# Kernel tuning notes

Measured on AMD Instinct MI355X. Metric: run time of the kernel, lower is better.

Reference implementation:

```python
import jax, jax.numpy as jnp
import numpy as np

B, T, DIM = 4, 2048, 64
NUM_CODES = 512

def setup_inputs() -> dict:
    key = jax.random.key(0)
    k1, k2 = jax.random.split(key)
    inputs = jax.random.normal(k1, (B, T, DIM), dtype=jnp.float32)
    # original init: truncated_normal(mean=0.5, stddev=0) -> constant 0.5; use
    # a real random codebook so argmin is non-degenerate, matching trained state
    lookup_table = jax.random.normal(k2, (NUM_CODES, DIM), dtype=jnp.float32)
    return {"inputs": inputs, "lookup_table": lookup_table}

def reference(inputs, lookup_table):
    # z: [B, T, 1, dim]; table: [1, 1, K, dim] -> diff [B, T, K, dim]
    diff = inputs[..., None, :] - lookup_table[None, None, :, :]
    dist = jnp.linalg.norm(diff, axis=-1)          # [B, T, K]
    k = jnp.argmin(dist, axis=-1)                  # [B, T] int
    z_q = jnp.take(lookup_table, k, axis=0)        # [B, T, dim]
    return (k, z_q)
```

## Files before the change

### kernel.cpp

```cpp
#include <hip/hip_runtime.h>
#include <math.h>


#define NQ      8192
#define VDIM    64
#define NCODES  512
#define QB      32
#define CB      32
#define NCHUNK  (NCODES / CB)

__global__ __launch_bounds__(64, 2) void vq_dist_kernel(
    const float* __restrict__ inp,
    const float* __restrict__ table,
    float* __restrict__ wnorm,
    int* __restrict__ widx)
{
    __shared__ float4 qt[QB * 16];
    __shared__ float4 ct[CB * 16];

    const int l  = threadIdx.x;
    const int bc = blockIdx.x & (NCHUNK - 1);
    const int bq = blockIdx.x >> 4;

    {
        const float4* gq = reinterpret_cast<const float4*>(inp   + (size_t)bq * QB * VDIM);
        const float4* gc = reinterpret_cast<const float4*>(table + (size_t)bc * CB * VDIM);
#pragma unroll
        for (int it = 0; it < 8; ++it) {
            int f  = l + it * 64;
            int r  = f >> 4;
            int kc = f & 15;
            int d  = r * 16 + (kc ^ ((r >> 2) & 7));
            qt[d] = gq[f];
            ct[d] = gc[f];
        }
    }
    __syncthreads();

    const int xq = l & 7;
    const int xc = l >> 3;
    const float4* qb = qt + xq * 4 * 16;
    const float4* cb = ct + xc * 4 * 16;

    float acc[4][4][8];
#pragma unroll
    for (int i = 0; i < 4; ++i)
#pragma unroll
        for (int j = 0; j < 4; ++j)
#pragma unroll
            for (int m = 0; m < 8; ++m) acc[i][j][m] = 0.0f;

#pragma clang loop unroll(disable)
    for (int k = 0; k < 8; ++k) {
        {
            const int kc = 2 * k;
            float4 qv[4], cv[4];
#pragma unroll
            for (int i = 0; i < 4; ++i) qv[i] = qb[i * 16 + (kc ^ xq)];
#pragma unroll
            for (int j = 0; j < 4; ++j) cv[j] = cb[j * 16 + (kc ^ xc)];
#pragma unroll
            for (int i = 0; i < 4; ++i)
#pragma unroll
                for (int j = 0; j < 4; ++j) {
                    float d0 = qv[i].x - cv[j].x;
                    float d1 = qv[i].y - cv[j].y;
                    float d2 = qv[i].z - cv[j].z;
                    float d3 = qv[i].w - cv[j].w;
                    acc[i][j][0] = __builtin_fmaf(d0, d0, acc[i][j][0]);
                    acc[i][j][1] = __builtin_fmaf(d1, d1, acc[i][j][1]);
                    acc[i][j][2] = __builtin_fmaf(d2, d2, acc[i][j][2]);
                    acc[i][j][3] = __builtin_fmaf(d3, d3, acc[i][j][3]);
                }
        }
        {
            const int kc = 2 * k + 1;
            float4 qv[4], cv[4];
#pragma unroll
            for (int i = 0; i < 4; ++i) qv[i] = qb[i * 16 + (kc ^ xq)];
#pragma unroll
            for (int j = 0; j < 4; ++j) cv[j] = cb[j * 16 + (kc ^ xc)];
#pragma unroll
            for (int i = 0; i < 4; ++i)
#pragma unroll
                for (int j = 0; j < 4; ++j) {
                    float d0 = qv[i].x - cv[j].x;
                    float d1 = qv[i].y - cv[j].y;
                    float d2 = qv[i].z - cv[j].z;
                    float d3 = qv[i].w - cv[j].w;
                    acc[i][j][4] = __builtin_fmaf(d0, d0, acc[i][j][4]);
                    acc[i][j][5] = __builtin_fmaf(d1, d1, acc[i][j][5]);
                    acc[i][j][6] = __builtin_fmaf(d2, d2, acc[i][j][6]);
                    acc[i][j][7] = __builtin_fmaf(d3, d3, acc[i][j][7]);
                }
        }
    }

    float bd[4];
    int   bi[4];
#pragma unroll
    for (int i = 0; i < 4; ++i) { bd[i] = INFINITY; bi[i] = 0; }
#pragma unroll
    for (int j = 0; j < 4; ++j) {
#pragma unroll
        for (int i = 0; i < 4; ++i) {
            float s = ((acc[i][j][0] + acc[i][j][1]) + (acc[i][j][2] + acc[i][j][3]))
                    + ((acc[i][j][4] + acc[i][j][5]) + (acc[i][j][6] + acc[i][j][7]));
            float n = sqrtf(s);
            if (n < bd[i]) { bd[i] = n; bi[i] = bc * CB + xc * 4 + j; }
        }
    }

#pragma unroll
    for (int off = 8; off < 64; off <<= 1) {
#pragma unroll
        for (int i = 0; i < 4; ++i) {
            float nd = __shfl_xor(bd[i], off, 64);
            int   ni = __shfl_xor(bi[i], off, 64);
            if (nd < bd[i] || (nd == bd[i] && ni < bi[i])) { bd[i] = nd; bi[i] = ni; }
        }
    }

    if (xc == 0) {
#pragma unroll
        for (int i = 0; i < 4; ++i) {
            wnorm[(size_t)bc * NQ + bq * QB + 4 * l + i] = bd[i];
            widx [(size_t)bc * NQ + bq * QB + 4 * l + i] = bi[i];
        }
    }
}

__global__ __launch_bounds__(256) void vq_finalize_kernel(
    const float* __restrict__ table,
    const float* __restrict__ wnorm,
    const int* __restrict__ widx,
    float* __restrict__ out)
{
    const int gid = blockIdx.x * 256 + threadIdx.x;
    const int q = gid >> 6;
    const int d = gid & 63;

    float best = INFINITY;
    int   bidx = 0;
#pragma unroll
    for (int p = 0; p < NCHUNK; ++p) {
        float n = wnorm[(size_t)p * NQ + q];
        int   i = widx [(size_t)p * NQ + q];
        if (n < best || (n == best && i < bidx)) { best = n; bidx = i; }
    }

    out[NQ + (size_t)q * VDIM + d] = table[(size_t)bidx * VDIM + d];
    if (d == 0) out[q] = (float)bidx;
}

extern "C" void kernel_launch(void* const* d_in, const int* in_sizes, int n_in,
                              void* d_out, int out_size, void* d_ws, size_t ws_size,
                              hipStream_t stream) {
    const float* inp   = (const float*)d_in[0];
    const float* table = (const float*)d_in[1];
    float* out = (float*)d_out;

    float* wnorm = (float*)d_ws;
    int*   widx  = (int*)(wnorm + (size_t)NCHUNK * NQ);

    vq_dist_kernel<<<dim3((NQ / QB) * NCHUNK), dim3(64), 0, stream>>>(inp, table, wnorm, widx);
    vq_finalize_kernel<<<dim3((NQ * VDIM) / 256), dim3(256), 0, stream>>>(table, wnorm, widx, out);
}
```

Baseline: 36.83 us.

## Fuse distance, argmin and gather into one kernel with in-block reduction

Replaces the two-kernel scheme (partial argmin per code chunk written to workspace, then a finalize kernel) with one kernel. Each block handles 16 queries across all 512 codes, split over 4 waves, and reduces the argmin through shuffles and shared memory before gathering codebook rows. This drops the workspace round trip and the second launch. In exchange, the LDS staging is gone and operands are read straight from global memory through cache. The grid also shrinks to 512 blocks, which lowers parallelism.

```diff
diff --git a/kernel.cpp b/kernel.cpp
--- a/kernel.cpp
+++ b/kernel.cpp
@@ -5,114 +5,107 @@
 #define NQ      8192
 #define VDIM    64
 #define NCODES  512
-#define QB      32
-#define CB      32
-#define NCHUNK  (NCODES / CB)
 
-__global__ __launch_bounds__(64, 2) void vq_dist_kernel(
+__global__ __launch_bounds__(256, 2) void vq_fused_kernel(
     const float* __restrict__ inp,
     const float* __restrict__ table,
-    float* __restrict__ wnorm,
-    int* __restrict__ widx)
+    float* __restrict__ out)
 {
-    __shared__ float4 qt[QB * 16];
-    __shared__ float4 ct[CB * 16];
+    __shared__ float red_n[4][16];
+    __shared__ int   red_i[4][16];
+    __shared__ int   kidx[16];
 
-    const int l  = threadIdx.x;
-    const int bc = blockIdx.x & (NCHUNK - 1);
-    const int bq = blockIdx.x >> 4;
+    const int tid  = threadIdx.x;
+    const int wave = tid >> 6;
+    const int lane = tid & 63;
+    const int qg   = lane >> 4;
+    const int cg   = lane & 15;
 
-    {
-        const float4* gq = reinterpret_cast<const float4*>(inp   + (size_t)bq * QB * VDIM);
-        const float4* gc = reinterpret_cast<const float4*>(table + (size_t)bc * CB * VDIM);
-#pragma unroll
-        for (int it = 0; it < 8; ++it) {
-            int f  = l + it * 64;
-            int r  = f >> 4;
-            int kc = f & 15;
-            int d  = r * 16 + (kc ^ ((r >> 2) & 7));
-            qt[d] = gq[f];
-            ct[d] = gc[f];
-        }
-    }
-    __syncthreads();
-
-    const int xq = l & 7;
-    const int xc = l >> 3;
-    const float4* qb = qt + xq * 4 * 16;
-    const float4* cb = ct + xc * 4 * 16;
-
-    float acc[4][4][8];
-#pragma unroll
-    for (int i = 0; i < 4; ++i)
-#pragma unroll
-        for (int j = 0; j < 4; ++j)
-#pragma unroll
-            for (int m = 0; m < 8; ++m) acc[i][j][m] = 0.0f;
-
-#pragma clang loop unroll(disable)
-    for (int k = 0; k < 8; ++k) {
-        {
-            const int kc = 2 * k;
-            float4 qv[4], cv[4];
-#pragma unroll
-            for (int i = 0; i < 4; ++i) qv[i] = qb[i * 16 + (kc ^ xq)];
-#pragma unroll
-            for (int j = 0; j < 4; ++j) cv[j] = cb[j * 16 + (kc ^ xc)];
-#pragma unroll
-            for (int i = 0; i < 4; ++i)
-#pragma unroll
-                for (int j = 0; j < 4; ++j) {
-                    float d0 = qv[i].x - cv[j].x;
-                    float d1 = qv[i].y - cv[j].y;
-                    float d2 = qv[i].z - cv[j].z;
-                    float d3 = qv[i].w - cv[j].w;
-                    acc[i][j][0] = __builtin_fmaf(d0, d0, acc[i][j][0]);
-                    acc[i][j][1] = __builtin_fmaf(d1, d1, acc[i][j][1]);
-                    acc[i][j][2] = __builtin_fmaf(d2, d2, acc[i][j][2]);
-                    acc[i][j][3] = __builtin_fmaf(d3, d3, acc[i][j][3]);
-                }
-        }
-        {
-            const int kc = 2 * k + 1;
-            float4 qv[4], cv[4];
-#pragma unroll
-            for (int i = 0; i < 4; ++i) qv[i] = qb[i * 16 + (kc ^ xq)];
-#pragma unroll
-            for (int j = 0; j < 4; ++j) cv[j] = cb[j * 16 + (kc ^ xc)];
-#pragma unroll
-            for (int i = 0; i < 4; ++i)
-#pragma unroll
-                for (int j = 0; j < 4; ++j) {
-                    float d0 = qv[i].x - cv[j].x;
-                    float d1 = qv[i].y - cv[j].y;
-                    float d2 = qv[i].z - cv[j].z;
-                    float d3 = qv[i].w - cv[j].w;
-                    acc[i][j][4] = __builtin_fmaf(d0, d0, acc[i][j][4]);
-                    acc[i][j][5] = __builtin_fmaf(d1, d1, acc[i][j][5]);
-                    acc[i][j][6] = __builtin_fmaf(d2, d2, acc[i][j][6]);
-                    acc[i][j][7] = __builtin_fmaf(d3, d3, acc[i][j][7]);
-                }
-        }
-    }
+    const int qbase = blockIdx.x * 16;
+    const float* qrow = inp + (size_t)(qbase + qg * 4) * VDIM;
 
     float bd[4];
     int   bi[4];
 #pragma unroll
     for (int i = 0; i < 4; ++i) { bd[i] = INFINITY; bi[i] = 0; }
+
+#pragma clang loop unroll(disable)
+    for (int chunk = 0; chunk < 2; ++chunk) {
+        const int cbase = wave * 128 + chunk * 64 + cg * 4;
+        const float* crow = table + (size_t)cbase * VDIM;
+
+        float acc[4][4][8];
 #pragma unroll
-    for (int j = 0; j < 4; ++j) {
+        for (int i = 0; i < 4; ++i)
 #pragma unroll
-        for (int i = 0; i < 4; ++i) {
-            float s = ((acc[i][j][0] + acc[i][j][1]) + (acc[i][j][2] + acc[i][j][3]))
-                    + ((acc[i][j][4] + acc[i][j][5]) + (acc[i][j][6] + acc[i][j][7]));
-            float n = sqrtf(s);
-            if (n < bd[i]) { bd[i] = n; bi[i] = bc * CB + xc * 4 + j; }
+            for (int j = 0; j < 4; ++j)
+#pragma unroll
+                for (int m = 0; m < 8; ++m) acc[i][j][m] = 0.0f;
+
+#pragma clang loop unroll(disable)
+        for (int k = 0; k < 8; ++k) {
+            {
+                const int kc = 2 * k;
+                float4 qv[4], cv[4];
+#pragma unroll
+                for (int i = 0; i < 4; ++i)
+                    qv[i] = *reinterpret_cast<const float4*>(qrow + i * VDIM + kc * 4);
+#pragma unroll
+                for (int j = 0; j < 4; ++j)
+                    cv[j] = *reinterpret_cast<const float4*>(crow + j * VDIM + kc * 4);
+#pragma unroll
+                for (int i = 0; i < 4; ++i)
+#pragma unroll
+                    for (int j = 0; j < 4; ++j) {
+                        float d0 = qv[i].x - cv[j].x;
+                        float d1 = qv[i].y - cv[j].y;
+                        float d2 = qv[i].z - cv[j].z;
+                        float d3 = qv[i].w - cv[j].w;
+                        acc[i][j][0] = __builtin_fmaf(d0, d0, acc[i][j][0]);
+                        acc[i][j][1] = __builtin_fmaf(d1, d1, acc[i][j][1]);
+                        acc[i][j][2] = __builtin_fmaf(d2, d2, acc[i][j][2]);
+                        acc[i][j][3] = __builtin_fmaf(d3, d3, acc[i][j][3]);
+                    }
+            }
+            {
+                const int kc = 2 * k + 1;
+                float4 qv[4], cv[4];
+#pragma unroll
+                for (int i = 0; i < 4; ++i)
+                    qv[i] = *reinterpret_cast<const float4*>(qrow + i * VDIM + kc * 4);
+#pragma unroll
+                for (int j = 0; j < 4; ++j)
+                    cv[j] = *reinterpret_cast<const float4*>(crow + j * VDIM + kc * 4);
+#pragma unroll
+                for (int i = 0; i < 4; ++i)
+#pragma unroll
+                    for (int j = 0; j < 4; ++j) {
+                        float d0 = qv[i].x - cv[j].x;
+                        float d1 = qv[i].y - cv[j].y;
+                        float d2 = qv[i].z - cv[j].z;
+                        float d3 = qv[i].w - cv[j].w;
+                        acc[i][j][4] = __builtin_fmaf(d0, d0, acc[i][j][4]);
+                        acc[i][j][5] = __builtin_fmaf(d1, d1, acc[i][j][5]);
+                        acc[i][j][6] = __builtin_fmaf(d2, d2, acc[i][j][6]);
+                        acc[i][j][7] = __builtin_fmaf(d3, d3, acc[i][j][7]);
+                    }
+            }
+        }
+
+#pragma unroll
+        for (int j = 0; j < 4; ++j) {
+#pragma unroll
+            for (int i = 0; i < 4; ++i) {
+                float s = ((acc[i][j][0] + acc[i][j][1]) + (acc[i][j][2] + acc[i][j][3]))
+                        + ((acc[i][j][4] + acc[i][j][5]) + (acc[i][j][6] + acc[i][j][7]));
+                float n = sqrtf(s);
+                if (n < bd[i]) { bd[i] = n; bi[i] = cbase + j; }
+            }
         }
     }
 
 #pragma unroll
-    for (int off = 8; off < 64; off <<= 1) {
+    for (int off = 1; off < 16; off <<= 1) {
 #pragma unroll
         for (int i = 0; i < 4; ++i) {
             float nd = __shfl_xor(bd[i], off, 64);
@@ -121,36 +114,37 @@
         }
     }
 
-    if (xc == 0) {
+    if (cg == 0) {
 #pragma unroll
         for (int i = 0; i < 4; ++i) {
-            wnorm[(size_t)bc * NQ + bq * QB + 4 * l + i] = bd[i];
-            widx [(size_t)bc * NQ + bq * QB + 4 * l + i] = bi[i];
+            red_n[wave][qg * 4 + i] = bd[i];
+            red_i[wave][qg * 4 + i] = bi[i];
         }
     }
-}
+    __syncthreads();
 
-__global__ __launch_bounds__(256) void vq_finalize_kernel(
-    const float* __restrict__ table,
-    const float* __restrict__ wnorm,
-    const int* __restrict__ widx,
-    float* __restrict__ out)
-{
-    const int gid = blockIdx.x * 256 + threadIdx.x;
-    const int q = gid >> 6;
-    const int d = gid & 63;
+    if (tid < 16) {
+        float best = INFINITY;
+        int   bidx = 0;
+#pragma unroll
+        for (int w = 0; w < 4; ++w) {
+            float n = red_n[w][tid];
+            int   i = red_i[w][tid];
+            if (n < best || (n == best && i < bidx)) { best = n; bidx = i; }
+        }
+        kidx[tid] = bidx;
+        out[qbase + tid] = (float)bidx;
+    }
+    __syncthreads();
 
-    float best = INFINITY;
-    int   bidx = 0;
 #pragma unroll
-    for (int p = 0; p < NCHUNK; ++p) {
-        float n = wnorm[(size_t)p * NQ + q];
-        int   i = widx [(size_t)p * NQ + q];
-        if (n < best || (n == best && i < bidx)) { best = n; bidx = i; }
+    for (int it = 0; it < 4; ++it) {
+        int flat = it * 256 + tid;
+        int ql = flat >> 6;
+        int d  = flat & 63;
+        int bidx = kidx[ql];
+        out[NQ + (size_t)(qbase + ql) * VDIM + d] = table[(size_t)bidx * VDIM + d];
     }
-
-    out[NQ + (size_t)q * VDIM + d] = table[(size_t)bidx * VDIM + d];
-    if (d == 0) out[q] = (float)bidx;
 }
 
 extern "C" void kernel_launch(void* const* d_in, const int* in_sizes, int n_in,
@@ -160,9 +154,5 @@
     const float* table = (const float*)d_in[1];
     float* out = (float*)d_out;
 
-    float* wnorm = (float*)d_ws;
-    int*   widx  = (int*)(wnorm + (size_t)NCHUNK * NQ);
-
-    vq_dist_kernel<<<dim3((NQ / QB) * NCHUNK), dim3(64), 0, stream>>>(inp, table, wnorm, widx);
-    vq_finalize_kernel<<<dim3((NQ * VDIM) / 256), dim3(256), 0, stream>>>(table, wnorm, widx, out);
+    vq_fused_kernel<<<dim3(NQ / 16), dim3(256), 0, stream>>>(inp, table, out);
 }
```

New measurement: 46.76 us. +27.0%, slower.
